# Performance work log

Measured on AMD Instinct MI355X. Metric: run time of the kernel, lower is better.

## Reference

```python
import jax, jax.numpy as jnp
import numpy as np

B, T, D, H = 8, 512, 1024, 16
DK = D // H  # 64
EPS = 1e-3  # Keras BatchNormalization default epsilon


def batchnorm(x, gamma, beta):
    # Keras BN over feature axis (-1), training-mode batch statistics over (B, T)
    mean = jnp.mean(x, axis=(0, 1), keepdims=True)
    var = jnp.var(x, axis=(0, 1), keepdims=True)
    return (x - mean) * jax.lax.rsqrt(var + EPS) * gamma + beta


def setup_inputs() -> dict:
    key = jax.random.key(0)
    ks = jax.random.split(key, 12)
    s = 0.05
    return {
        "x": jax.random.normal(ks[0], (B, T, D), dtype=jnp.float32),
        "Wq": jax.random.uniform(ks[1], (H, D, DK), dtype=jnp.float32, minval=-s, maxval=s),
        "Wk": jax.random.uniform(ks[2], (H, D, DK), dtype=jnp.float32, minval=-s, maxval=s),
        "Wv": jax.random.uniform(ks[3], (H, D, DK), dtype=jnp.float32, minval=-s, maxval=s),
        "W": jax.random.uniform(ks[4], (D, D), dtype=jnp.float32, minval=-s, maxval=s),
        "W1": jax.random.normal(ks[5], (D, D), dtype=jnp.float32) * 0.02,
        "b1": jnp.zeros((D,), dtype=jnp.float32),
        "W2": jax.random.normal(ks[6], (D, D), dtype=jnp.float32) * 0.02,
        "b2": jnp.zeros((D,), dtype=jnp.float32),
        "g1": jnp.ones((D,), dtype=jnp.float32),
        "be1": jnp.zeros((D,), dtype=jnp.float32),
        "g2": jnp.ones((D,), dtype=jnp.float32),
        "be2": jnp.zeros((D,), dtype=jnp.float32),
    }


def reference(x, Wq, Wk, Wv, W, W1, b1, W2, b2, g1, be1, g2, be2):
    # Batched multi-head attention (replaces the per-head Python loop)
    q = jnp.einsum("btd,hdk->bhtk", x, Wq)
    k = jnp.einsum("btd,hdk->bhtk", x, Wk)
    v = jnp.einsum("btd,hdk->bhtk", x, Wv)
    scores = jnp.einsum("bhtk,bhsk->bhts", q, k) / jnp.sqrt(jnp.float32(DK))
    w = jax.nn.softmax(scores, axis=-1)
    attn = jnp.einsum("bhts,bhsk->bhtk", w, v)
    # concat heads: [B,H,T,DK] -> [B,T,H*DK] (head-major concat order as in the loop)
    concat = jnp.transpose(attn, (0, 2, 1, 3)).reshape(B, T, D)
    out = concat @ W
    out1 = batchnorm(x + out, g1, be1)
    out2 = jax.nn.relu(out1 @ W1 + b1) @ W2 + b2
    return batchnorm(out1 + out2, g2, be2)
```

## Files before the change

### kernel.cpp

```cpp
#include <hip/hip_runtime.h>
#include <hip/hip_bf16.h>
#include <cstdint>

#define Bn 8
#define Tn 512
#define Dn 1024
#define Hn 16
#define DKn 64
#define Mn (Bn * Tn)

typedef unsigned short u16;
typedef short bf16x8 __attribute__((ext_vector_type(8)));
typedef float f32x4 __attribute__((ext_vector_type(4)));

__device__ __forceinline__ u16 f2bf(float f) {
  unsigned int u = __builtin_bit_cast(unsigned int, f);
  u += 0x7fffu + ((u >> 16) & 1u);
  return (u16)(u >> 16);
}
__device__ __forceinline__ unsigned int pack2bf(float lo, float hi) {
  return (unsigned int)f2bf(lo) | ((unsigned int)f2bf(hi) << 16);
}

__device__ __forceinline__ void gl2lds16(const void* g, void* l) {
  __builtin_amdgcn_global_load_lds(
      (const __attribute__((address_space(1))) unsigned int*)g,
      (__attribute__((address_space(3))) unsigned int*)l,
      16, 0, 0);
}

__device__ __forceinline__ void hard_barrier() {
  __builtin_amdgcn_sched_barrier(0);
  __builtin_amdgcn_s_barrier();
  __builtin_amdgcn_sched_barrier(0);
}
#define WAITV(n_) asm volatile("s_waitcnt vmcnt(" #n_ ")" ::: "memory")

__global__ __launch_bounds__(256) void cvt_bf16_k(
    const float* __restrict__ src, u16* __restrict__ dst)
{
  const size_t i = ((size_t)blockIdx.x * 256 + threadIdx.x) * 8;
  float4 a = *reinterpret_cast<const float4*>(&src[i]);
  float4 b = *reinterpret_cast<const float4*>(&src[i + 4]);
  uint4 w;
  w.x = pack2bf(a.x, a.y); w.y = pack2bf(a.z, a.w);
  w.z = pack2bf(b.x, b.y); w.w = pack2bf(b.z, b.w);
  *reinterpret_cast<uint4*>(&dst[i]) = w;
}

__global__ __launch_bounds__(256) void tqkv_k(
    const float* __restrict__ wq, const float* __restrict__ wk,
    const float* __restrict__ wv, u16* __restrict__ dst)
{
  const int kt = blockIdx.x;
  const int y  = blockIdx.y;
  const int tau = y >> 4, head = y & 15;
  const float* src = (tau == 0 ? wq : tau == 1 ? wk : wv) + (size_t)head * 65536;
  const int t = threadIdx.x;
  const int n  = t & 63;
  const int kq = (t >> 6) << 4;
  const int k0 = kt << 6;
  u16 v[16];
#pragma unroll
  for (int j = 0; j < 16; j++)
    v[j] = f2bf(src[(size_t)(k0 + kq + j) * 64 + n]);
  u16* d = &dst[((size_t)tau * 1024 + head * 64 + n) * 1024 + k0 + kq];
  *reinterpret_cast<uint4*>(&d[0]) = *reinterpret_cast<uint4*>(&v[0]);
  *reinterpret_cast<uint4*>(&d[8]) = *reinterpret_cast<uint4*>(&v[8]);
}

__global__ __launch_bounds__(256) void tw_k(
    const float* __restrict__ W, const float* __restrict__ W1,
    const float* __restrict__ W2, u16* __restrict__ wt,
    u16* __restrict__ w1t, u16* __restrict__ w2t)
{
  const int kt = blockIdx.x, ntl = blockIdx.y, z = blockIdx.z;
  const float* src = (z == 0 ? W : z == 1 ? W1 : W2);
  u16* dst = (z == 0 ? wt : z == 1 ? w1t : w2t);
  const int t = threadIdx.x;
  const int n  = (ntl << 6) + (t & 63);
  const int kq = (t >> 6) << 4;
  const int k0 = kt << 6;
  u16 v[16];
#pragma unroll
  for (int j = 0; j < 16; j++)
    v[j] = f2bf(src[(size_t)(k0 + kq + j) * 1024 + n]);
  u16* d = &dst[(size_t)n * 1024 + k0 + kq];
  *reinterpret_cast<uint4*>(&d[0]) = *reinterpret_cast<uint4*>(&v[0]);
  *reinterpret_cast<uint4*>(&d[8]) = *reinterpret_cast<uint4*>(&v[8]);
}

template<int BIAS, int RELU, int OUTM, int RES, int VT, int RESNORM>
__global__ __launch_bounds__(512) void mgemm_k(
    const u16* __restrict__ A, const u16* __restrict__ Bt,
    const float* __restrict__ bias,
    float* __restrict__ Cf, u16* __restrict__ Cb, int ldc,
    const float* __restrict__ Rres, float* __restrict__ Rout,
    float* __restrict__ psum, float* __restrict__ psumsq,
    u16* __restrict__ Vt,
    const float* __restrict__ nsc, const float* __restrict__ nsh)
{
  __shared__ __align__(16) u16 As[3][4096];
  __shared__ __align__(16) u16 Bs[3][4096];

  const int nwg = gridDim.x * gridDim.y;
  const int fid = blockIdx.y * gridDim.x + blockIdx.x;
  const int lid = (fid & 7) * (nwg >> 3) + (fid >> 3);
  const int bx = lid % gridDim.x, by = lid / gridDim.x;

  const int tid  = threadIdx.x;
  const int lane = tid & 63;
  const int wid  = tid >> 6;
  const int wm = wid >> 2, wn = wid & 3;
  const int g4 = lane >> 4, r15 = lane & 15;
  const int m0 = by << 7, n0 = bx << 7;

  const int srow  = tid >> 2;
  const int sslot = tid & 3;
  const int ssw   = (srow ^ (srow >> 2)) & 3;
  const int sk8   = ((sslot ^ ssw) << 3);
  const u16* ga0 = &A[(size_t)(m0 + srow) * 1024 + sk8];
  const u16* gb0 = &Bt[(size_t)(n0 + srow) * 1024 + sk8];
  const int lofs = wid * 1024;

  f32x4 acc[4][2] = {};

  auto stage_t = [&](int t, int bofs) {
    gl2lds16(ga0 + t * 32, (char*)As + bofs + lofs);
    gl2lds16(gb0 + t * 32, (char*)Bs + bofs + lofs);
  };
  auto compute_t = [&](int bofs) {
    bf16x8 af[4], bfr[2];
#pragma unroll
    for (int m = 0; m < 4; m++) {
      int row = wm * 64 + m * 16 + r15;
      int sw = (row ^ (row >> 2)) & 3;
      af[m] = *reinterpret_cast<const bf16x8*>(
          (const char*)As + bofs + row * 64 + ((g4 ^ sw) << 4));
    }
#pragma unroll
    for (int n = 0; n < 2; n++) {
      int row = wn * 32 + n * 16 + r15;
      int sw = (row ^ (row >> 2)) & 3;
      bfr[n] = *reinterpret_cast<const bf16x8*>(
          (const char*)Bs + bofs + row * 64 + ((g4 ^ sw) << 4));
    }
#pragma unroll
    for (int m = 0; m < 4; m++)
#pragma unroll
      for (int n = 0; n < 2; n++)
        acc[m][n] = __builtin_amdgcn_mfma_f32_16x16x32_bf16(af[m], bfr[n], acc[m][n], 0, 0, 0);
  };

  stage_t(0, 0);
  stage_t(1, 8192);

  int rd = 0, wr = 2;
#pragma unroll 1
  for (int t = 0; t < 30; ++t) {
    stage_t(t + 2, wr * 8192);
    WAITV(4);
    hard_barrier();
    compute_t(rd * 8192);
    hard_barrier();
    wr = rd;
    rd = (rd + 1 == 3) ? 0 : rd + 1;
  }
  WAITV(2);
  hard_barrier();
  compute_t(0);
  hard_barrier();
  WAITV(0);
  hard_barrier();
  compute_t(8192);

  if (VT && bx >= 16) {
    const int vcol0 = n0 - 2048;
#pragma unroll
    for (int m = 0; m < 4; m++) {
      int row0 = m0 + wm * 64 + m * 16 + g4 * 4;
      int bI = row0 >> 9, s = row0 & 511;
#pragma unroll
      for (int n = 0; n < 2; n++) {
        int cv = vcol0 + wn * 32 + n * 16 + r15;
        int hh = cv >> 6, dk = cv & 63;
        uint2 pk;
        pk.x = pack2bf(acc[m][n][0], acc[m][n][1]);
        pk.y = pack2bf(acc[m][n][2], acc[m][n][3]);
        *reinterpret_cast<uint2*>(
            &Vt[(((size_t)(bI * 16 + hh) * 64 + dk) << 9) + s]) = pk;
      }
    }
    return;
  }

  float bb[2] = {0.f, 0.f};
  if (BIAS) {
#pragma unroll
    for (int n = 0; n < 2; n++) bb[n] = bias[n0 + wn * 32 + n * 16 + r15];
  }

  if (RES) {
    float sc_[2], sh_[2];
    if (RESNORM) {
#pragma unroll
      for (int n = 0; n < 2; n++) {
        int col = n0 + wn * 32 + n * 16 + r15;
        sc_[n] = nsc[col];
        sh_[n] = nsh[col];
      }
    }
    float sp[2] = {0.f, 0.f}, sq[2] = {0.f, 0.f};
#pragma unroll
    for (int m = 0; m < 4; m++) {
      int row = m0 + wm * 64 + m * 16 + g4 * 4;
#pragma unroll
      for (int n = 0; n < 2; n++) {
        int col = n0 + wn * 32 + n * 16 + r15;
#pragma unroll
        for (int j = 0; j < 4; j++) {
          float v = acc[m][n][j] + bb[n];
          float res = Rres[(size_t)(row + j) * 1024 + col];
          if (RESNORM) res = fmaf(res, sc_[n], sh_[n]);
          float r = v + res;
          Rout[(size_t)(row + j) * 1024 + col] = r;
          sp[n] += r;
          sq[n] = fmaf(r, r, sq[n]);
        }
      }
    }
#pragma unroll
    for (int n = 0; n < 2; n++) {
      sp[n] += __shfl_xor(sp[n], 16, 64);
      sp[n] += __shfl_xor(sp[n], 32, 64);
      sq[n] += __shfl_xor(sq[n], 16, 64);
      sq[n] += __shfl_xor(sq[n], 32, 64);
    }
    if (g4 == 0) {
      int slot = (by << 1) + wm;
#pragma unroll
      for (int n = 0; n < 2; n++) {
        int col = n0 + wn * 32 + n * 16 + r15;
        psum[(size_t)slot * 1024 + col] = sp[n];
        psumsq[(size_t)slot * 1024 + col] = sq[n];
      }
    }
    return;
  }

#pragma unroll
  for (int m = 0; m < 4; m++) {
    int row = m0 + wm * 64 + m * 16 + g4 * 4;
#pragma unroll
    for (int n = 0; n < 2; n++) {
      int col = n0 + wn * 32 + n * 16 + r15;
#pragma unroll
      for (int j = 0; j < 4; j++) {
        float v = acc[m][n][j];
        if (BIAS) v += bb[n];
        if (RELU) v = fmaxf(v, 0.f);
        if (OUTM == 1)      Cb[(size_t)(row + j) * ldc + col] = f2bf(v);
        else if (OUTM == 0) Cf[(size_t)(row + j) * ldc + col] = v;
      }
    }
  }
}

__global__ __launch_bounds__(256, 2) void attn_k(
    const u16* __restrict__ qk, const u16* __restrict__ Vt,
    u16* __restrict__ o)
{
  __shared__ __align__(16) unsigned char Ks[2][16384];
  __shared__ __align__(16) unsigned char Vs[2][16384];
  __shared__ __align__(16) unsigned char Ps[16384];

  const int bh  = blockIdx.x;
  const int qc  = blockIdx.y;
  const int b   = bh >> 4, h = bh & 15;
  const int tid = threadIdx.x;
  const int lane = tid & 63;
  const int wv   = tid >> 6;
  const int qcol = lane & 15;
  const int g    = lane >> 4;

  const size_t rowbase = (size_t)b * Tn;
  const size_t qrow0   = rowbase + qc * 64 + wv * 16;

  bf16x8 qf[2];
  {
    const u16* qp = &qk[(qrow0 + qcol) * 2048 + h * 64 + g * 8];
    qf[0] = *reinterpret_cast<const bf16x8*>(qp);
    qf[1] = *reinterpret_cast<const bf16x8*>(qp + 32);
  }

  f32x4 oa[4] = {};
  float m_run = -3e38f, l_run = 0.f;

  const int krow = tid >> 3, kch = tid & 7;
  const int vrow = tid >> 4, vch = tid & 15;
  unsigned char* Pw = &Ps[wv * 4096];

  auto stage_kv = [&](int c, int buf) {
#pragma unroll
    for (int i = 0; i < 4; i++) {
      int row = i * 32 + krow;
      const u16* gk = &qk[(rowbase + c * 128 + row) * 2048 + 1024 + h * 64
                          + ((kch ^ (row & 7)) << 3)];
      gl2lds16(gk, (char*)Ks[buf] + wv * 1024 + i * 4096);
    }
#pragma unroll
    for (int i = 0; i < 4; i++) {
      int row = i * 16 + vrow;
      const u16* gv = &Vt[(((size_t)bh * 64 + row) << 9) + c * 128
                          + ((vch ^ (row & 7)) << 3)];
      gl2lds16(gv, (char*)Vs[buf] + wv * 1024 + i * 4096);
    }
  };

  auto compute_c = [&](int cur) {
    f32x4 sf[8];
#pragma unroll
    for (int t = 0; t < 8; t++) {
      sf[t] = (f32x4){0.f, 0.f, 0.f, 0.f};
      const int srow = t * 16 + qcol;
      const int base = srow * 128;
      const int sw = srow & 7;
#pragma unroll
      for (int ks = 0; ks < 2; ks++) {
        bf16x8 a = *reinterpret_cast<const bf16x8*>(
            &Ks[cur][base + (((ks * 4 + g) ^ sw) << 4)]);
        sf[t] = __builtin_amdgcn_mfma_f32_16x16x32_bf16(a, qf[ks], sf[t], 0, 0, 0);
      }
    }

    float mc = -3e38f;
#pragma unroll
    for (int t = 0; t < 8; t++)
#pragma unroll
      for (int r = 0; r < 4; r++) {
        float s = sf[t][r] * 0.125f;
        sf[t][r] = s;
        mc = fmaxf(mc, s);
      }
    mc = fmaxf(mc, __shfl_xor(mc, 16, 64));
    mc = fmaxf(mc, __shfl_xor(mc, 32, 64));
    float mnew = fmaxf(m_run, mc);
    float alpha = __expf(m_run - mnew);
    m_run = mnew;

    float lsum = 0.f;
#pragma unroll
    for (int t = 0; t < 8; t++)
#pragma unroll
      for (int r = 0; r < 4; r++) {
        float e = __expf(sf[t][r] - mnew);
        sf[t][r] = e;
        lsum += e;
      }
    lsum += __shfl_xor(lsum, 16, 64);
    lsum += __shfl_xor(lsum, 32, 64);
    l_run = l_run * alpha + lsum;

#pragma unroll
    for (int j = 0; j < 4; j++) {
      float av = __shfl(alpha, (g << 4) + g * 4 + j, 64);
#pragma unroll
      for (int nt = 0; nt < 4; nt++) oa[nt][j] *= av;
    }

#pragma unroll
    for (int t = 0; t < 8; t++) {
      int o0 = t * 32 + g * 8;
      int chunk = o0 >> 4;
      int sb = ((chunk ^ (qcol & 7)) << 4) | (o0 & 15);
      *reinterpret_cast<unsigned int*>(&Pw[qcol * 256 + sb]) =
          pack2bf(sf[t][0], sf[t][1]);
      *reinterpret_cast<unsigned int*>(&Pw[qcol * 256 + sb + 4]) =
          pack2bf(sf[t][2], sf[t][3]);
    }

    bf16x8 pa[4];
#pragma unroll
    for (int ks = 0; ks < 4; ks++)
      pa[ks] = *reinterpret_cast<const bf16x8*>(
          &Pw[qcol * 256 + (((ks * 4 + g) ^ (qcol & 7)) << 4)]);
#pragma unroll
    for (int nt = 0; nt < 4; nt++) {
      const int vr = nt * 16 + qcol;
      const int vsw = vr & 7;
#pragma unroll
      for (int ks = 0; ks < 4; ks++) {
        bf16x8 bvf = *reinterpret_cast<const bf16x8*>(
            &Vs[cur][vr * 256 + (((ks * 4 + g) ^ vsw) << 4)]);
        oa[nt] = __builtin_amdgcn_mfma_f32_16x16x32_bf16(pa[ks], bvf, oa[nt], 0, 0, 0);
      }
    }
  };

  stage_kv(0, 0);
#pragma unroll 1
  for (int c = 0; c < 3; ++c) {
    stage_kv(c + 1, (c + 1) & 1);
    WAITV(8);
    hard_barrier();
    compute_c(c & 1);
    hard_barrier();
  }
  WAITV(0);
  hard_barrier();
  compute_c(1);

  float rl = 1.f / l_run;
#pragma unroll
  for (int j = 0; j < 4; j++) {
    float il = __shfl(rl, (g << 4) + g * 4 + j, 64);
#pragma unroll
    for (int nt = 0; nt < 4; nt++)
      o[(qrow0 + g * 4 + j) * 1024 + h * 64 + nt * 16 + qcol] =
          f2bf(oa[nt][j] * il);
  }
}

__global__ __launch_bounds__(256) void reduce_stats_k(
    const float* __restrict__ ps, const float* __restrict__ pq,
    const float* __restrict__ g, const float* __restrict__ be,
    float* __restrict__ scale, float* __restrict__ shift)
{
  const int col = blockIdx.x * 256 + threadIdx.x;
  float s = 0.f, q = 0.f;
  for (int p = 0; p < 64; p++) {
    s += ps[(size_t)p * Dn + col];
    q += pq[(size_t)p * Dn + col];
  }
  const float invn = 1.f / 4096.f;
  float mean = s * invn;
  float var = q * invn - mean * mean;
  float inv = rsqrtf(var + 1e-3f);
  float sc = g[col] * inv;
  scale[col] = sc;
  shift[col] = be[col] - mean * sc;
}

template<int OUTMODE>
__global__ __launch_bounds__(256) void norm_k(
    const float* __restrict__ r, const float* __restrict__ scale,
    const float* __restrict__ shift, float* __restrict__ o, u16* __restrict__ ob)
{
  const size_t idx = (size_t)blockIdx.x * 256 + threadIdx.x;
  const int c4 = ((int)idx & 255) << 2;
  float4 rv = *reinterpret_cast<const float4*>(&r[idx << 2]);
  float4 sc = *reinterpret_cast<const float4*>(&scale[c4]);
  float4 sh = *reinterpret_cast<const float4*>(&shift[c4]);
  float4 ov = make_float4(fmaf(rv.x, sc.x, sh.x), fmaf(rv.y, sc.y, sh.y),
                          fmaf(rv.z, sc.z, sh.z), fmaf(rv.w, sc.w, sh.w));
  if (OUTMODE == 0) {
    *reinterpret_cast<float4*>(&o[idx << 2]) = ov;
  } else {
    uint2 p;
    p.x = pack2bf(ov.x, ov.y);
    p.y = pack2bf(ov.z, ov.w);
    *reinterpret_cast<uint2*>(&ob[idx << 2]) = p;
  }
}

extern "C" void kernel_launch(void* const* d_in, const int* in_sizes, int n_in,
                              void* d_out, int out_size, void* d_ws, size_t ws_size,
                              hipStream_t stream)
{
  const float* x   = (const float*)d_in[0];
  const float* wq  = (const float*)d_in[1];
  const float* wk  = (const float*)d_in[2];
  const float* wv  = (const float*)d_in[3];
  const float* W   = (const float*)d_in[4];
  const float* W1  = (const float*)d_in[5];
  const float* b1  = (const float*)d_in[6];
  const float* W2  = (const float*)d_in[7];
  const float* b2  = (const float*)d_in[8];
  const float* g1  = (const float*)d_in[9];
  const float* be1 = (const float*)d_in[10];
  const float* g2  = (const float*)d_in[11];
  const float* be2 = (const float*)d_in[12];

  float* out = (float*)d_out;
  float* ws  = (float*)d_ws;

  const size_t NB = (size_t)Mn * Dn;
  float* ws1    = ws;
  float* ws2    = ws1 + NB;
  float* psum   = ws2 + NB;
  float* psumsq = psum + 64 * Dn;
  float* scale1 = psumsq + 64 * Dn;
  float* shift1 = scale1 + Dn;
  float* scale2 = shift1 + Dn;
  float* shift2 = scale2 + Dn;
  u16* xb      = (u16*)(shift2 + Dn);
  u16* qkb     = xb + NB;
  u16* vtb     = qkb + 2 * NB;
  u16* concatb = vtb + NB;
  u16* wqkvT   = concatb + NB;
  u16* wt      = wqkvT + 3 * 1048576;
  u16* w1t     = wt + 1048576;
  u16* w2t     = w1t + 1048576;
  u16* out1b = qkb;
  u16* hb    = qkb + NB;

  dim3 b256(256), b512(512);

  cvt_bf16_k<<<dim3(2048), b256, 0, stream>>>(x, xb);
  tqkv_k<<<dim3(16, 48), b256, 0, stream>>>(wq, wk, wv, wqkvT);
  tw_k<<<dim3(16, 16, 3), b256, 0, stream>>>(W, W1, W2, wt, w1t, w2t);

  mgemm_k<0, 0, 1, 0, 1, 0><<<dim3(24, 32), b512, 0, stream>>>(
      xb, wqkvT, nullptr, nullptr, qkb, 2048,
      nullptr, nullptr, nullptr, nullptr, vtb, nullptr, nullptr);
  attn_k<<<dim3(128, 8), b256, 0, stream>>>(qkb, vtb, concatb);
  mgemm_k<0, 0, 2, 1, 0, 0><<<dim3(8, 32), b512, 0, stream>>>(
      concatb, wt, nullptr, nullptr, nullptr, 1024,
      x, ws1, psum, psumsq, nullptr, nullptr, nullptr);
  reduce_stats_k<<<dim3(4), b256, 0, stream>>>(psum, psumsq, g1, be1, scale1, shift1);
  norm_k<2><<<dim3(NB / 1024), b256, 0, stream>>>(ws1, scale1, shift1, nullptr, out1b);
  mgemm_k<1, 1, 1, 0, 0, 0><<<dim3(8, 32), b512, 0, stream>>>(
      out1b, w1t, b1, nullptr, hb, 1024,
      nullptr, nullptr, nullptr, nullptr, nullptr, nullptr, nullptr);
  mgemm_k<1, 0, 2, 1, 0, 1><<<dim3(8, 32), b512, 0, stream>>>(
      hb, w2t, b2, nullptr, nullptr, 1024,
      ws1, ws2, psum, psumsq, nullptr, scale1, shift1);
  reduce_stats_k<<<dim3(4), b256, 0, stream>>>(psum, psumsq, g2, be2, scale2, shift2);
  norm_k<0><<<dim3(NB / 1024), b256, 0, stream>>>(ws2, scale2, shift2, out, nullptr);
}
```

Measured before the change: 171.9 us.

## Use 4-wave 64x64 warp tiles in GEMM and merge prep kernels

The GEMM kernel drops from 8 waves to 4 waves per 128x128 block. Each wave now computes a 64x64 sub-tile with 16 MFMA accumulators instead of 32 columns, and each thread issues two global-to-LDS loads per operand per stage. This raises MFMA work per LDS fragment read, at the cost of more registers per thread and fewer waves to hide latency. Separately, the three weight and input conversion kernels are merged into a single launch to cut launch overhead.

```diff
diff --git a/kernel.cpp b/kernel.cpp
--- a/kernel.cpp
+++ b/kernel.cpp
@@ -36,62 +36,62 @@
 }
 #define WAITV(n_) asm volatile("s_waitcnt vmcnt(" #n_ ")" ::: "memory")
 
-__global__ __launch_bounds__(256) void cvt_bf16_k(
-    const float* __restrict__ src, u16* __restrict__ dst)
-{
-  const size_t i = ((size_t)blockIdx.x * 256 + threadIdx.x) * 8;
-  float4 a = *reinterpret_cast<const float4*>(&src[i]);
-  float4 b = *reinterpret_cast<const float4*>(&src[i + 4]);
-  uint4 w;
-  w.x = pack2bf(a.x, a.y); w.y = pack2bf(a.z, a.w);
-  w.z = pack2bf(b.x, b.y); w.w = pack2bf(b.z, b.w);
-  *reinterpret_cast<uint4*>(&dst[i]) = w;
-}
-
-__global__ __launch_bounds__(256) void tqkv_k(
+__global__ __launch_bounds__(256) void prep_k(
+    const float* __restrict__ x, u16* __restrict__ xb,
     const float* __restrict__ wq, const float* __restrict__ wk,
-    const float* __restrict__ wv, u16* __restrict__ dst)
-{
-  const int kt = blockIdx.x;
-  const int y  = blockIdx.y;
-  const int tau = y >> 4, head = y & 15;
-  const float* src = (tau == 0 ? wq : tau == 1 ? wk : wv) + (size_t)head * 65536;
-  const int t = threadIdx.x;
-  const int n  = t & 63;
-  const int kq = (t >> 6) << 4;
-  const int k0 = kt << 6;
-  u16 v[16];
-#pragma unroll
-  for (int j = 0; j < 16; j++)
-    v[j] = f2bf(src[(size_t)(k0 + kq + j) * 64 + n]);
-  u16* d = &dst[((size_t)tau * 1024 + head * 64 + n) * 1024 + k0 + kq];
-  *reinterpret_cast<uint4*>(&d[0]) = *reinterpret_cast<uint4*>(&v[0]);
-  *reinterpret_cast<uint4*>(&d[8]) = *reinterpret_cast<uint4*>(&v[8]);
-}
-
-__global__ __launch_bounds__(256) void tw_k(
+    const float* __restrict__ wv, u16* __restrict__ wqkvT,
     const float* __restrict__ W, const float* __restrict__ W1,
     const float* __restrict__ W2, u16* __restrict__ wt,
     u16* __restrict__ w1t, u16* __restrict__ w2t)
 {
-  const int kt = blockIdx.x, ntl = blockIdx.y, z = blockIdx.z;
-  const float* src = (z == 0 ? W : z == 1 ? W1 : W2);
-  u16* dst = (z == 0 ? wt : z == 1 ? w1t : w2t);
+  const int bid = blockIdx.x;
   const int t = threadIdx.x;
-  const int n  = (ntl << 6) + (t & 63);
-  const int kq = (t >> 6) << 4;
-  const int k0 = kt << 6;
-  u16 v[16];
-#pragma unroll
-  for (int j = 0; j < 16; j++)
-    v[j] = f2bf(src[(size_t)(k0 + kq + j) * 1024 + n]);
-  u16* d = &dst[(size_t)n * 1024 + k0 + kq];
-  *reinterpret_cast<uint4*>(&d[0]) = *reinterpret_cast<uint4*>(&v[0]);
-  *reinterpret_cast<uint4*>(&d[8]) = *reinterpret_cast<uint4*>(&v[8]);
+  if (bid < 2048) {
+    const size_t i = ((size_t)bid * 256 + t) * 8;
+    float4 a = *reinterpret_cast<const float4*>(&x[i]);
+    float4 b = *reinterpret_cast<const float4*>(&x[i + 4]);
+    uint4 w;
+    w.x = pack2bf(a.x, a.y); w.y = pack2bf(a.z, a.w);
+    w.z = pack2bf(b.x, b.y); w.w = pack2bf(b.z, b.w);
+    *reinterpret_cast<uint4*>(&xb[i]) = w;
+  } else if (bid < 2816) {
+    const int idx = bid - 2048;
+    const int kt = idx & 15;
+    const int y  = idx >> 4;
+    const int tau = y >> 4, head = y & 15;
+    const float* src = (tau == 0 ? wq : tau == 1 ? wk : wv) + (size_t)head * 65536;
+    const int n  = t & 63;
+    const int kq = (t >> 6) << 4;
+    const int k0 = kt << 6;
+    u16 v[16];
+#pragma unroll
+    for (int j = 0; j < 16; j++)
+      v[j] = f2bf(src[(size_t)(k0 + kq + j) * 64 + n]);
+    u16* d = &wqkvT[((size_t)tau * 1024 + head * 64 + n) * 1024 + k0 + kq];
+    *reinterpret_cast<uint4*>(&d[0]) = *reinterpret_cast<uint4*>(&v[0]);
+    *reinterpret_cast<uint4*>(&d[8]) = *reinterpret_cast<uint4*>(&v[8]);
+  } else {
+    const int idx = bid - 2816;
+    const int kt = idx & 15;
+    const int rest = idx >> 4;
+    const int ntl = rest & 15, z = rest >> 4;
+    const float* src = (z == 0 ? W : z == 1 ? W1 : W2);
+    u16* dst = (z == 0 ? wt : z == 1 ? w1t : w2t);
+    const int n  = (ntl << 6) + (t & 63);
+    const int kq = (t >> 6) << 4;
+    const int k0 = kt << 6;
+    u16 v[16];
+#pragma unroll
+    for (int j = 0; j < 16; j++)
+      v[j] = f2bf(src[(size_t)(k0 + kq + j) * 1024 + n]);
+    u16* d = &dst[(size_t)n * 1024 + k0 + kq];
+    *reinterpret_cast<uint4*>(&d[0]) = *reinterpret_cast<uint4*>(&v[0]);
+    *reinterpret_cast<uint4*>(&d[8]) = *reinterpret_cast<uint4*>(&v[8]);
+  }
 }
 
 template<int BIAS, int RELU, int OUTM, int RES, int VT, int RESNORM>
-__global__ __launch_bounds__(512) void mgemm_k(
+__global__ __launch_bounds__(256) void mgemm_k(
     const u16* __restrict__ A, const u16* __restrict__ Bt,
     const float* __restrict__ bias,
     float* __restrict__ Cf, u16* __restrict__ Cb, int ldc,
@@ -111,26 +111,35 @@
   const int tid  = threadIdx.x;
   const int lane = tid & 63;
   const int wid  = tid >> 6;
-  const int wm = wid >> 2, wn = wid & 3;
+  const int wm = wid >> 1, wn = wid & 1;
   const int g4 = lane >> 4, r15 = lane & 15;
   const int m0 = by << 7, n0 = bx << 7;
 
-  const int srow  = tid >> 2;
+  const int srow2 = tid >> 2;
   const int sslot = tid & 3;
-  const int ssw   = (srow ^ (srow >> 2)) & 3;
-  const int sk8   = ((sslot ^ ssw) << 3);
-  const u16* ga0 = &A[(size_t)(m0 + srow) * 1024 + sk8];
-  const u16* gb0 = &Bt[(size_t)(n0 + srow) * 1024 + sk8];
-  const int lofs = wid * 1024;
-
-  f32x4 acc[4][2] = {};
+  const u16* gaP[2]; const u16* gbP[2];
+#pragma unroll
+  for (int i = 0; i < 2; i++) {
+    int row = i * 64 + srow2;
+    int ssw = (row ^ (row >> 2)) & 3;
+    int sk8 = ((sslot ^ ssw) << 3);
+    gaP[i] = &A[(size_t)(m0 + row) * 1024 + sk8];
+    gbP[i] = &Bt[(size_t)(n0 + row) * 1024 + sk8];
+  }
+  const int dofs = wid * 1024;
+
+  f32x4 acc[4][4] = {};
 
   auto stage_t = [&](int t, int bofs) {
-    gl2lds16(ga0 + t * 32, (char*)As + bofs + lofs);
-    gl2lds16(gb0 + t * 32, (char*)Bs + bofs + lofs);
+#pragma unroll
+    for (int i = 0; i < 2; i++)
+      gl2lds16(gaP[i] + t * 32, (char*)As + bofs + i * 4096 + dofs);
+#pragma unroll
+    for (int i = 0; i < 2; i++)
+      gl2lds16(gbP[i] + t * 32, (char*)Bs + bofs + i * 4096 + dofs);
   };
   auto compute_t = [&](int bofs) {
-    bf16x8 af[4], bfr[2];
+    bf16x8 af[4], bfr[4];
 #pragma unroll
     for (int m = 0; m < 4; m++) {
       int row = wm * 64 + m * 16 + r15;
@@ -139,8 +148,8 @@
           (const char*)As + bofs + row * 64 + ((g4 ^ sw) << 4));
     }
 #pragma unroll
-    for (int n = 0; n < 2; n++) {
-      int row = wn * 32 + n * 16 + r15;
+    for (int n = 0; n < 4; n++) {
+      int row = wn * 64 + n * 16 + r15;
       int sw = (row ^ (row >> 2)) & 3;
       bfr[n] = *reinterpret_cast<const bf16x8*>(
           (const char*)Bs + bofs + row * 64 + ((g4 ^ sw) << 4));
@@ -148,7 +157,7 @@
 #pragma unroll
     for (int m = 0; m < 4; m++)
 #pragma unroll
-      for (int n = 0; n < 2; n++)
+      for (int n = 0; n < 4; n++)
         acc[m][n] = __builtin_amdgcn_mfma_f32_16x16x32_bf16(af[m], bfr[n], acc[m][n], 0, 0, 0);
   };
 
@@ -159,14 +168,14 @@
 #pragma unroll 1
   for (int t = 0; t < 30; ++t) {
     stage_t(t + 2, wr * 8192);
-    WAITV(4);
+    WAITV(8);
     hard_barrier();
     compute_t(rd * 8192);
     hard_barrier();
     wr = rd;
     rd = (rd + 1 == 3) ? 0 : rd + 1;
   }
-  WAITV(2);
+  WAITV(4);
   hard_barrier();
   compute_t(0);
   hard_barrier();
@@ -181,8 +190,8 @@
       int row0 = m0 + wm * 64 + m * 16 + g4 * 4;
       int bI = row0 >> 9, s = row0 & 511;
 #pragma unroll
-      for (int n = 0; n < 2; n++) {
-        int cv = vcol0 + wn * 32 + n * 16 + r15;
+      for (int n = 0; n < 4; n++) {
+        int cv = vcol0 + wn * 64 + n * 16 + r15;
         int hh = cv >> 6, dk = cv & 63;
         uint2 pk;
         pk.x = pack2bf(acc[m][n][0], acc[m][n][1]);
@@ -194,29 +203,29 @@
     return;
   }
 
-  float bb[2] = {0.f, 0.f};
+  float bb[4] = {0.f, 0.f, 0.f, 0.f};
   if (BIAS) {
 #pragma unroll
-    for (int n = 0; n < 2; n++) bb[n] = bias[n0 + wn * 32 + n * 16 + r15];
+    for (int n = 0; n < 4; n++) bb[n] = bias[n0 + wn * 64 + n * 16 + r15];
   }
 
   if (RES) {
-    float sc_[2], sh_[2];
+    float sc_[4], sh_[4];
     if (RESNORM) {
 #pragma unroll
-      for (int n = 0; n < 2; n++) {
-        int col = n0 + wn * 32 + n * 16 + r15;
+      for (int n = 0; n < 4; n++) {
+        int col = n0 + wn * 64 + n * 16 + r15;
         sc_[n] = nsc[col];
         sh_[n] = nsh[col];
       }
     }
-    float sp[2] = {0.f, 0.f}, sq[2] = {0.f, 0.f};
+    float sp[4] = {0.f, 0.f, 0.f, 0.f}, sq[4] = {0.f, 0.f, 0.f, 0.f};
 #pragma unroll
     for (int m = 0; m < 4; m++) {
       int row = m0 + wm * 64 + m * 16 + g4 * 4;
 #pragma unroll
-      for (int n = 0; n < 2; n++) {
-        int col = n0 + wn * 32 + n * 16 + r15;
+      for (int n = 0; n < 4; n++) {
+        int col = n0 + wn * 64 + n * 16 + r15;
 #pragma unroll
         for (int j = 0; j < 4; j++) {
           float v = acc[m][n][j] + bb[n];
@@ -230,7 +239,7 @@
       }
     }
 #pragma unroll
-    for (int n = 0; n < 2; n++) {
+    for (int n = 0; n < 4; n++) {
       sp[n] += __shfl_xor(sp[n], 16, 64);
       sp[n] += __shfl_xor(sp[n], 32, 64);
       sq[n] += __shfl_xor(sq[n], 16, 64);
@@ -239,8 +248,8 @@
     if (g4 == 0) {
       int slot = (by << 1) + wm;
 #pragma unroll
-      for (int n = 0; n < 2; n++) {
-        int col = n0 + wn * 32 + n * 16 + r15;
+      for (int n = 0; n < 4; n++) {
+        int col = n0 + wn * 64 + n * 16 + r15;
         psum[(size_t)slot * 1024 + col] = sp[n];
         psumsq[(size_t)slot * 1024 + col] = sq[n];
       }
@@ -252,8 +261,8 @@
   for (int m = 0; m < 4; m++) {
     int row = m0 + wm * 64 + m * 16 + g4 * 4;
 #pragma unroll
-    for (int n = 0; n < 2; n++) {
-      int col = n0 + wn * 32 + n * 16 + r15;
+    for (int n = 0; n < 4; n++) {
+      int col = n0 + wn * 64 + n * 16 + r15;
 #pragma unroll
       for (int j = 0; j < 4; j++) {
         float v = acc[m][n][j];
@@ -504,25 +513,24 @@
   u16* out1b = qkb;
   u16* hb    = qkb + NB;
 
-  dim3 b256(256), b512(512);
-
-  cvt_bf16_k<<<dim3(2048), b256, 0, stream>>>(x, xb);
-  tqkv_k<<<dim3(16, 48), b256, 0, stream>>>(wq, wk, wv, wqkvT);
-  tw_k<<<dim3(16, 16, 3), b256, 0, stream>>>(W, W1, W2, wt, w1t, w2t);
-
-  mgemm_k<0, 0, 1, 0, 1, 0><<<dim3(24, 32), b512, 0, stream>>>(
+  dim3 b256(256);
+
+  prep_k<<<dim3(3584), b256, 0, stream>>>(x, xb, wq, wk, wv, wqkvT,
+                                          W, W1, W2, wt, w1t, w2t);
+
+  mgemm_k<0, 0, 1, 0, 1, 0><<<dim3(24, 32), b256, 0, stream>>>(
       xb, wqkvT, nullptr, nullptr, qkb, 2048,
       nullptr, nullptr, nullptr, nullptr, vtb, nullptr, nullptr);
   attn_k<<<dim3(128, 8), b256, 0, stream>>>(qkb, vtb, concatb);
-  mgemm_k<0, 0, 2, 1, 0, 0><<<dim3(8, 32), b512, 0, stream>>>(
+  mgemm_k<0, 0, 2, 1, 0, 0><<<dim3(8, 32), b256, 0, stream>>>(
       concatb, wt, nullptr, nullptr, nullptr, 1024,
       x, ws1, psum, psumsq, nullptr, nullptr, nullptr);
   reduce_stats_k<<<dim3(4), b256, 0, stream>>>(psum, psumsq, g1, be1, scale1, shift1);
   norm_k<2><<<dim3(NB / 1024), b256, 0, stream>>>(ws1, scale1, shift1, nullptr, out1b);
-  mgemm_k<1, 1, 1, 0, 0, 0><<<dim3(8, 32), b512, 0, stream>>>(
+  mgemm_k<1, 1, 1, 0, 0, 0><<<dim3(8, 32), b256, 0, stream>>>(
       out1b, w1t, b1, nullptr, hb, 1024,
       nullptr, nullptr, nullptr, nullptr, nullptr, nullptr, nullptr);
-  mgemm_k<1, 0, 2, 1, 0, 1><<<dim3(8, 32), b512, 0, stream>>>(
+  mgemm_k<1, 0, 2, 1, 0, 1><<<dim3(8, 32), b256, 0, stream>>>(
       hb, w2t, b2, nullptr, nullptr, 1024,
       ws1, ws2, psum, psumsq, nullptr, scale1, shift1);
   reduce_stats_k<<<dim3(4), b256, 0, stream>>>(psum, psumsq, g2, be2, scale2, shift2);
```

Result: slower. 194.2 us (+13.0%).

## Use 64-row GEMM tiles for D×D GEMMs and merge prep kernels

Applied to the files above, without the earlier changes.

Adds a 64x128-tile GEMM variant for the three 1024-wide GEMMs, doubling the grid from 256 to 512 workgroups so the 256 CUs are better filled. The BN partial-sum buffers and reduction grow from 64 to 128 row blocks to match. The three weight/input conversion kernels are fused into one launch, saving launch overhead. Smaller tiles lower per-block data reuse and add more partial-stat traffic.

```diff
diff --git a/kernel.cpp b/kernel.cpp
--- a/kernel.cpp
+++ b/kernel.cpp
@@ -36,69 +36,64 @@
 }
 #define WAITV(n_) asm volatile("s_waitcnt vmcnt(" #n_ ")" ::: "memory")
 
-__global__ __launch_bounds__(256) void cvt_bf16_k(
-    const float* __restrict__ src, u16* __restrict__ dst)
-{
-  const size_t i = ((size_t)blockIdx.x * 256 + threadIdx.x) * 8;
-  float4 a = *reinterpret_cast<const float4*>(&src[i]);
-  float4 b = *reinterpret_cast<const float4*>(&src[i + 4]);
-  uint4 w;
-  w.x = pack2bf(a.x, a.y); w.y = pack2bf(a.z, a.w);
-  w.z = pack2bf(b.x, b.y); w.w = pack2bf(b.z, b.w);
-  *reinterpret_cast<uint4*>(&dst[i]) = w;
-}
-
-__global__ __launch_bounds__(256) void tqkv_k(
+__global__ __launch_bounds__(256) void prep_k(
+    const float* __restrict__ x, u16* __restrict__ xb,
     const float* __restrict__ wq, const float* __restrict__ wk,
-    const float* __restrict__ wv, u16* __restrict__ dst)
-{
-  const int kt = blockIdx.x;
-  const int y  = blockIdx.y;
-  const int tau = y >> 4, head = y & 15;
-  const float* src = (tau == 0 ? wq : tau == 1 ? wk : wv) + (size_t)head * 65536;
-  const int t = threadIdx.x;
-  const int n  = t & 63;
-  const int kq = (t >> 6) << 4;
-  const int k0 = kt << 6;
-  u16 v[16];
-#pragma unroll
-  for (int j = 0; j < 16; j++)
-    v[j] = f2bf(src[(size_t)(k0 + kq + j) * 64 + n]);
-  u16* d = &dst[((size_t)tau * 1024 + head * 64 + n) * 1024 + k0 + kq];
-  *reinterpret_cast<uint4*>(&d[0]) = *reinterpret_cast<uint4*>(&v[0]);
-  *reinterpret_cast<uint4*>(&d[8]) = *reinterpret_cast<uint4*>(&v[8]);
-}
-
-__global__ __launch_bounds__(256) void tw_k(
+    const float* __restrict__ wv, u16* __restrict__ wqkvT,
     const float* __restrict__ W, const float* __restrict__ W1,
     const float* __restrict__ W2, u16* __restrict__ wt,
     u16* __restrict__ w1t, u16* __restrict__ w2t)
 {
-  const int kt = blockIdx.x, ntl = blockIdx.y, z = blockIdx.z;
-  const float* src = (z == 0 ? W : z == 1 ? W1 : W2);
-  u16* dst = (z == 0 ? wt : z == 1 ? w1t : w2t);
+  const int bid = blockIdx.x;
   const int t = threadIdx.x;
-  const int n  = (ntl << 6) + (t & 63);
-  const int kq = (t >> 6) << 4;
-  const int k0 = kt << 6;
-  u16 v[16];
-#pragma unroll
-  for (int j = 0; j < 16; j++)
-    v[j] = f2bf(src[(size_t)(k0 + kq + j) * 1024 + n]);
-  u16* d = &dst[(size_t)n * 1024 + k0 + kq];
-  *reinterpret_cast<uint4*>(&d[0]) = *reinterpret_cast<uint4*>(&v[0]);
-  *reinterpret_cast<uint4*>(&d[8]) = *reinterpret_cast<uint4*>(&v[8]);
-}
-
-template<int BIAS, int RELU, int OUTM, int RES, int VT, int RESNORM>
+  if (bid < 2048) {
+    const size_t i = ((size_t)bid * 256 + t) * 8;
+    float4 a = *reinterpret_cast<const float4*>(&x[i]);
+    float4 b = *reinterpret_cast<const float4*>(&x[i + 4]);
+    uint4 w;
+    w.x = pack2bf(a.x, a.y); w.y = pack2bf(a.z, a.w);
+    w.z = pack2bf(b.x, b.y); w.w = pack2bf(b.z, b.w);
+    *reinterpret_cast<uint4*>(&xb[i]) = w;
+  } else if (bid < 2816) {
+    const int idx = bid - 2048;
+    const int kt = idx & 15;
+    const int y  = idx >> 4;
+    const int tau = y >> 4, head = y & 15;
+    const float* src = (tau == 0 ? wq : tau == 1 ? wk : wv) + (size_t)head * 65536;
+    const int n  = t & 63;
+    const int kq = (t >> 6) << 4;
+    const int k0 = kt << 6;
+    u16 v[16];
+#pragma unroll
+    for (int j = 0; j < 16; j++)
+      v[j] = f2bf(src[(size_t)(k0 + kq + j) * 64 + n]);
+    u16* d = &wqkvT[((size_t)tau * 1024 + head * 64 + n) * 1024 + k0 + kq];
+    *reinterpret_cast<uint4*>(&d[0]) = *reinterpret_cast<uint4*>(&v[0]);
+    *reinterpret_cast<uint4*>(&d[8]) = *reinterpret_cast<uint4*>(&v[8]);
+  } else {
+    const int idx = bid - 2816;
+    const int kt = idx & 15;
+    const int rest = idx >> 4;
+    const int ntl = rest & 15, z = rest >> 4;
+    const float* src = (z == 0 ? W : z == 1 ? W1 : W2);
+    u16* dst = (z == 0 ? wt : z == 1 ? w1t : w2t);
+    const int n  = (ntl << 6) + (t & 63);
+    const int kq = (t >> 6) << 4;
+    const int k0 = kt << 6;
+    u16 v[16];
+#pragma unroll
+    for (int j = 0; j < 16; j++)
+      v[j] = f2bf(src[(size_t)(k0 + kq + j) * 1024 + n]);
+    u16* d = &dst[(size_t)n * 1024 + k0 + kq];
+    *reinterpret_cast<uint4*>(&d[0]) = *reinterpret_cast<uint4*>(&v[0]);
+    *reinterpret_cast<uint4*>(&d[8]) = *reinterpret_cast<uint4*>(&v[8]);
+  }
+}
+
+template<int VT>
 __global__ __launch_bounds__(512) void mgemm_k(
     const u16* __restrict__ A, const u16* __restrict__ Bt,
-    const float* __restrict__ bias,
-    float* __restrict__ Cf, u16* __restrict__ Cb, int ldc,
-    const float* __restrict__ Rres, float* __restrict__ Rout,
-    float* __restrict__ psum, float* __restrict__ psumsq,
-    u16* __restrict__ Vt,
-    const float* __restrict__ nsc, const float* __restrict__ nsh)
+    u16* __restrict__ Cb, int ldc, u16* __restrict__ Vt)
 {
   __shared__ __align__(16) u16 As[3][4096];
   __shared__ __align__(16) u16 Bs[3][4096];
@@ -125,25 +120,25 @@
 
   f32x4 acc[4][2] = {};
 
-  auto stage_t = [&](int t, int bofs) {
-    gl2lds16(ga0 + t * 32, (char*)As + bofs + lofs);
-    gl2lds16(gb0 + t * 32, (char*)Bs + bofs + lofs);
+  auto stage_t = [&](int t, int buf) {
+    gl2lds16(ga0 + t * 32, (char*)As[buf] + lofs);
+    gl2lds16(gb0 + t * 32, (char*)Bs[buf] + lofs);
   };
-  auto compute_t = [&](int bofs) {
+  auto compute_t = [&](int buf) {
     bf16x8 af[4], bfr[2];
 #pragma unroll
     for (int m = 0; m < 4; m++) {
       int row = wm * 64 + m * 16 + r15;
       int sw = (row ^ (row >> 2)) & 3;
       af[m] = *reinterpret_cast<const bf16x8*>(
-          (const char*)As + bofs + row * 64 + ((g4 ^ sw) << 4));
+          (const char*)As[buf] + row * 64 + ((g4 ^ sw) << 4));
     }
 #pragma unroll
     for (int n = 0; n < 2; n++) {
       int row = wn * 32 + n * 16 + r15;
       int sw = (row ^ (row >> 2)) & 3;
       bfr[n] = *reinterpret_cast<const bf16x8*>(
-          (const char*)Bs + bofs + row * 64 + ((g4 ^ sw) << 4));
+          (const char*)Bs[buf] + row * 64 + ((g4 ^ sw) << 4));
     }
 #pragma unroll
     for (int m = 0; m < 4; m++)
@@ -153,15 +148,15 @@
   };
 
   stage_t(0, 0);
-  stage_t(1, 8192);
+  stage_t(1, 1);
 
   int rd = 0, wr = 2;
 #pragma unroll 1
   for (int t = 0; t < 30; ++t) {
-    stage_t(t + 2, wr * 8192);
+    stage_t(t + 2, wr);
     WAITV(4);
     hard_barrier();
-    compute_t(rd * 8192);
+    compute_t(rd);
     hard_barrier();
     wr = rd;
     rd = (rd + 1 == 3) ? 0 : rd + 1;
@@ -172,7 +167,7 @@
   hard_barrier();
   WAITV(0);
   hard_barrier();
-  compute_t(8192);
+  compute_t(1);
 
   if (VT && bx >= 16) {
     const int vcol0 = n0 - 2048;
@@ -194,6 +189,103 @@
     return;
   }
 
+#pragma unroll
+  for (int m = 0; m < 4; m++) {
+    int row = m0 + wm * 64 + m * 16 + g4 * 4;
+#pragma unroll
+    for (int n = 0; n < 2; n++) {
+      int col = n0 + wn * 32 + n * 16 + r15;
+#pragma unroll
+      for (int j = 0; j < 4; j++)
+        Cb[(size_t)(row + j) * ldc + col] = f2bf(acc[m][n][j]);
+    }
+  }
+}
+
+template<int BIAS, int RELU, int OUTM, int RES, int RESNORM>
+__global__ __launch_bounds__(512) void mgemm64_k(
+    const u16* __restrict__ A, const u16* __restrict__ Bt,
+    const float* __restrict__ bias, u16* __restrict__ Cb,
+    const float* __restrict__ Rres, float* __restrict__ Rout,
+    float* __restrict__ psum, float* __restrict__ psumsq,
+    const float* __restrict__ nsc, const float* __restrict__ nsh)
+{
+  __shared__ __align__(16) u16 As[3][2048];
+  __shared__ __align__(16) u16 Bs[3][4096];
+
+  const int nwg = gridDim.x * gridDim.y;
+  const int fid = blockIdx.y * gridDim.x + blockIdx.x;
+  const int lid = (fid & 7) * (nwg >> 3) + (fid >> 3);
+  const int bx = lid % gridDim.x, by = lid / gridDim.x;
+
+  const int tid  = threadIdx.x;
+  const int lane = tid & 63;
+  const int wid  = tid >> 6;
+  const int wm = wid >> 2, wn = wid & 3;
+  const int g4 = lane >> 4, r15 = lane & 15;
+  const int m0 = by << 6, n0 = bx << 7;
+
+  const int srow  = lane >> 2;
+  const int sslot = lane & 3;
+  const int arow  = (wid & 3) * 16 + srow;
+  const int asw   = (arow ^ (arow >> 2)) & 3;
+  const u16* gaP  = &A[(size_t)(m0 + arow) * 1024 + ((sslot ^ asw) << 3)];
+  const int brow  = wid * 16 + srow;
+  const int bsw   = (brow ^ (brow >> 2)) & 3;
+  const u16* gbP  = &Bt[(size_t)(n0 + brow) * 1024 + ((sslot ^ bsw) << 3)];
+
+  f32x4 acc[2][2] = {};
+
+  auto stage_t = [&](int t, int buf) {
+    if (wid < 4)
+      gl2lds16(gaP + t * 32, (char*)As[buf] + (wid & 3) * 1024);
+    gl2lds16(gbP + t * 32, (char*)Bs[buf] + wid * 1024);
+  };
+  auto compute_t = [&](int buf) {
+    bf16x8 af[2], bfr[2];
+#pragma unroll
+    for (int m = 0; m < 2; m++) {
+      int row = wm * 32 + m * 16 + r15;
+      int sw = (row ^ (row >> 2)) & 3;
+      af[m] = *reinterpret_cast<const bf16x8*>(
+          (const char*)As[buf] + row * 64 + ((g4 ^ sw) << 4));
+    }
+#pragma unroll
+    for (int n = 0; n < 2; n++) {
+      int row = wn * 32 + n * 16 + r15;
+      int sw = (row ^ (row >> 2)) & 3;
+      bfr[n] = *reinterpret_cast<const bf16x8*>(
+          (const char*)Bs[buf] + row * 64 + ((g4 ^ sw) << 4));
+    }
+#pragma unroll
+    for (int m = 0; m < 2; m++)
+#pragma unroll
+      for (int n = 0; n < 2; n++)
+        acc[m][n] = __builtin_amdgcn_mfma_f32_16x16x32_bf16(af[m], bfr[n], acc[m][n], 0, 0, 0);
+  };
+
+  stage_t(0, 0);
+  stage_t(1, 1);
+
+  int rd = 0, wr = 2;
+#pragma unroll 1
+  for (int t = 0; t < 30; ++t) {
+    stage_t(t + 2, wr);
+    if (wid < 4) { WAITV(4); } else { WAITV(2); }
+    hard_barrier();
+    compute_t(rd);
+    hard_barrier();
+    wr = rd;
+    rd = (rd + 1 == 3) ? 0 : rd + 1;
+  }
+  if (wid < 4) { WAITV(2); } else { WAITV(1); }
+  hard_barrier();
+  compute_t(0);
+  hard_barrier();
+  WAITV(0);
+  hard_barrier();
+  compute_t(1);
+
   float bb[2] = {0.f, 0.f};
   if (BIAS) {
 #pragma unroll
@@ -212,8 +304,8 @@
     }
     float sp[2] = {0.f, 0.f}, sq[2] = {0.f, 0.f};
 #pragma unroll
-    for (int m = 0; m < 4; m++) {
-      int row = m0 + wm * 64 + m * 16 + g4 * 4;
+    for (int m = 0; m < 2; m++) {
+      int row = m0 + wm * 32 + m * 16 + g4 * 4;
 #pragma unroll
       for (int n = 0; n < 2; n++) {
         int col = n0 + wn * 32 + n * 16 + r15;
@@ -249,8 +341,8 @@
   }
 
 #pragma unroll
-  for (int m = 0; m < 4; m++) {
-    int row = m0 + wm * 64 + m * 16 + g4 * 4;
+  for (int m = 0; m < 2; m++) {
+    int row = m0 + wm * 32 + m * 16 + g4 * 4;
 #pragma unroll
     for (int n = 0; n < 2; n++) {
       int col = n0 + wn * 32 + n * 16 + r15;
@@ -259,8 +351,7 @@
         float v = acc[m][n][j];
         if (BIAS) v += bb[n];
         if (RELU) v = fmaxf(v, 0.f);
-        if (OUTM == 1)      Cb[(size_t)(row + j) * ldc + col] = f2bf(v);
-        else if (OUTM == 0) Cf[(size_t)(row + j) * ldc + col] = v;
+        if (OUTM == 1) Cb[(size_t)(row + j) * 1024 + col] = f2bf(v);
       }
     }
   }
@@ -428,7 +519,7 @@
 {
   const int col = blockIdx.x * 256 + threadIdx.x;
   float s = 0.f, q = 0.f;
-  for (int p = 0; p < 64; p++) {
+  for (int p = 0; p < 128; p++) {
     s += ps[(size_t)p * Dn + col];
     q += pq[(size_t)p * Dn + col];
   }
@@ -488,8 +579,8 @@
   float* ws1    = ws;
   float* ws2    = ws1 + NB;
   float* psum   = ws2 + NB;
-  float* psumsq = psum + 64 * Dn;
-  float* scale1 = psumsq + 64 * Dn;
+  float* psumsq = psum + 128 * Dn;
+  float* scale1 = psumsq + 128 * Dn;
   float* shift1 = scale1 + Dn;
   float* scale2 = shift1 + Dn;
   float* shift2 = scale2 + Dn;
@@ -506,25 +597,18 @@
 
   dim3 b256(256), b512(512);
 
-  cvt_bf16_k<<<dim3(2048), b256, 0, stream>>>(x, xb);
-  tqkv_k<<<dim3(16, 48), b256, 0, stream>>>(wq, wk, wv, wqkvT);
-  tw_k<<<dim3(16, 16, 3), b256, 0, stream>>>(W, W1, W2, wt, w1t, w2t);
-
-  mgemm_k<0, 0, 1, 0, 1, 0><<<dim3(24, 32), b512, 0, stream>>>(
-      xb, wqkvT, nullptr, nullptr, qkb, 2048,
-      nullptr, nullptr, nullptr, nullptr, vtb, nullptr, nullptr);
+  prep_k<<<dim3(3584), b256, 0, stream>>>(x, xb, wq, wk, wv, wqkvT,
+                                          W, W1, W2, wt, w1t, w2t);
+  mgemm_k<1><<<dim3(24, 32), b512, 0, stream>>>(xb, wqkvT, qkb, 2048, vtb);
   attn_k<<<dim3(128, 8), b256, 0, stream>>>(qkb, vtb, concatb);
-  mgemm_k<0, 0, 2, 1, 0, 0><<<dim3(8, 32), b512, 0, stream>>>(
-      concatb, wt, nullptr, nullptr, nullptr, 1024,
-      x, ws1, psum, psumsq, nullptr, nullptr, nullptr);
+  mgemm64_k<0, 0, 2, 1, 0><<<dim3(8, 64), b512, 0, stream>>>(
+      concatb, wt, nullptr, nullptr, x, ws1, psum, psumsq, nullptr, nullptr);
   reduce_stats_k<<<dim3(4), b256, 0, stream>>>(psum, psumsq, g1, be1, scale1, shift1);
   norm_k<2><<<dim3(NB / 1024), b256, 0, stream>>>(ws1, scale1, shift1, nullptr, out1b);
-  mgemm_k<1, 1, 1, 0, 0, 0><<<dim3(8, 32), b512, 0, stream>>>(
-      out1b, w1t, b1, nullptr, hb, 1024,
-      nullptr, nullptr, nullptr, nullptr, nullptr, nullptr, nullptr);
-  mgemm_k<1, 0, 2, 1, 0, 1><<<dim3(8, 32), b512, 0, stream>>>(
-      hb, w2t, b2, nullptr, nullptr, 1024,
-      ws1, ws2, psum, psumsq, nullptr, scale1, shift1);
+  mgemm64_k<1, 1, 1, 0, 0><<<dim3(8, 64), b512, 0, stream>>>(
+      out1b, w1t, b1, hb, nullptr, nullptr, nullptr, nullptr, nullptr, nullptr);
+  mgemm64_k<1, 0, 2, 1, 1><<<dim3(8, 64), b512, 0, stream>>>(
+      hb, w2t, b2, nullptr, ws1, ws2, psum, psumsq, scale1, shift1);
   reduce_stats_k<<<dim3(4), b256, 0, stream>>>(psum, psumsq, g2, be2, scale2, shift2);
   norm_k<0><<<dim3(NB / 1024), b256, 0, stream>>>(ws2, scale2, shift2, out, nullptr);
 }
```

New measurement: 175.8 us. 1.02x slower.
